# Optimization experiments

Hardware: AMD Instinct MI355X
Metric: run time of the kernel (lower is better)

The kernel has to match this reference:

```python
import jax, jax.numpy as jnp
import numpy as np

B, QL, KVL = 4, 512, 4096
Q_DIM, KV_DIM = 1024, 768
QK_CH, V_CH, H = 1024, 1024, 8
DQK, DV = QK_CH // H, V_CH // H
LN_EPS = 1e-3  # keras LayerNormalization default epsilon


def layernorm(x, gamma, beta):
    mu = jnp.mean(x, axis=-1, keepdims=True)
    var = jnp.mean(jnp.square(x - mu), axis=-1, keepdims=True)
    return (x - mu) * jax.lax.rsqrt(var + LN_EPS) * gamma + beta


def setup_inputs() -> dict:
    key = jax.random.key(0)
    ks = jax.random.split(key, 8)
    s_q = 1.0 / np.sqrt(Q_DIM)
    s_kv = 1.0 / np.sqrt(KV_DIM)
    return {
        "hidden_states": jax.random.normal(ks[0], (B, QL, Q_DIM), jnp.float32),
        "inputs": jax.random.normal(ks[1], (B, KVL, KV_DIM), jnp.float32),
        "ln1_g": jnp.ones((Q_DIM,), jnp.float32),
        "ln1_b": jnp.zeros((Q_DIM,), jnp.float32),
        "ln2_g": jnp.ones((KV_DIM,), jnp.float32),
        "ln2_b": jnp.zeros((KV_DIM,), jnp.float32),
        "Wq": jax.random.normal(ks[2], (Q_DIM, QK_CH), jnp.float32) * s_q,
        "bq": jnp.zeros((QK_CH,), jnp.float32),
        "Wk": jax.random.normal(ks[3], (KV_DIM, QK_CH), jnp.float32) * s_kv,
        "bk": jnp.zeros((QK_CH,), jnp.float32),
        "Wv": jax.random.normal(ks[4], (KV_DIM, V_CH), jnp.float32) * s_kv,
        "bv": jnp.zeros((V_CH,), jnp.float32),
    }


def reference(hidden_states, inputs, ln1_g, ln1_b, ln2_g, ln2_b, Wq, bq, Wk, bk, Wv, bv):
    # LayerNorm latents and inputs (cross-attention path)
    hs = layernorm(hidden_states, ln1_g, ln1_b)   # [B, QL, Q_DIM]
    inp = layernorm(inputs, ln2_g, ln2_b)         # [B, KVL, KV_DIM]

    q = hs @ Wq + bq                               # [B, QL, QK_CH]
    k = inp @ Wk + bk                              # [B, KVL, QK_CH]
    v = inp @ Wv + bv                              # [B, KVL, V_CH]

    q = q.reshape(B, QL, H, DQK)
    k = k.reshape(B, KVL, H, DQK)
    v = v.reshape(B, KVL, H, DV)

    scores = jnp.einsum("bqhd,bkhd->bhqk", q, k) / jnp.sqrt(jnp.asarray(DQK, q.dtype))
    probs = jax.nn.softmax(scores, axis=-1)        # [B, H, QL, KVL]
    ctx = jnp.einsum("bhqk,bkhd->bqhd", probs, v)  # [B, QL, H, DV]
    return ctx.reshape(B, QL, H * DV)
```

## Files before the change

kernel.cpp:

```cpp
#include <hip/hip_runtime.h>
#include <hip/hip_bf16.h>
#include <stdint.h>

#define B_    4
#define QL_   512
#define KVL_  4096
#define QDIM  1024
#define KVDIM 768
#define NCH   1024
#define H_    8
#define DH    128
#define NROWS (B_ * H_ * QL_)
#define KVBLK 64
#define NS    4

typedef unsigned short ushort_t;
typedef __attribute__((ext_vector_type(8))) short bf16x8;
typedef __attribute__((ext_vector_type(4))) float f32x4;
typedef __attribute__((ext_vector_type(4))) unsigned short us4;

__device__ __forceinline__ ushort_t f2bf(float x){
  union { float f; unsigned u; } v; v.f = x;
  unsigned r = v.u + 0x7FFF + ((v.u >> 16) & 1);
  return (ushort_t)(r >> 16);
}

__device__ __forceinline__ float bf2f(unsigned hs){
  union { unsigned u; float f; } v; v.u = hs << 16; return v.f;
}

__device__ __forceinline__ void gload16(void* l, const void* g){
  __builtin_amdgcn_global_load_lds(
    (const __attribute__((address_space(1))) unsigned int*)g,
    (__attribute__((address_space(3))) unsigned int*)l, 16, 0, 0);
}

template<int D>
__global__ void ln_kernel(const float* __restrict__ x, const float* __restrict__ gamma,
                          const float* __restrict__ beta, ushort_t* __restrict__ out){
  constexpr int NW = D / 256;
  int row = blockIdx.x;
  const f32x4* xr = (const f32x4*)(x + (size_t)row * D);
  int tid = threadIdx.x;
  f32x4 v = xr[tid];
  float s  = v[0] + v[1] + v[2] + v[3];
  float s2 = v[0]*v[0] + v[1]*v[1] + v[2]*v[2] + v[3]*v[3];
  #pragma unroll
  for (int m = 32; m; m >>= 1){ s += __shfl_xor(s, m); s2 += __shfl_xor(s2, m); }
  __shared__ float red[2 * NW];
  int w = tid >> 6;
  if ((tid & 63) == 0){ red[w] = s; red[NW + w] = s2; }
  __syncthreads();
  s = 0.f; s2 = 0.f;
  #pragma unroll
  for (int i = 0; i < NW; ++i){ s += red[i]; s2 += red[NW + i]; }
  float mu  = s / D;
  float var = s2 / D - mu * mu;
  float rs  = rsqrtf(var + 1e-3f);
  f32x4 gm = ((const f32x4*)gamma)[tid];
  f32x4 bt = ((const f32x4*)beta)[tid];
  us4 o;
  #pragma unroll
  for (int e = 0; e < 4; ++e) o[e] = f2bf((v[e] - mu) * rs * gm[e] + bt[e]);
  ((us4*)(out + (size_t)row * D))[tid] = o;
}

__global__ void wtrans_kernel(const float* __restrict__ W, ushort_t* __restrict__ Wt,
                              int K, int N){
  __shared__ float t[32][33];
  int n0 = blockIdx.x * 32, k0 = blockIdx.y * 32;
  int tx = threadIdx.x & 31, ty = threadIdx.x >> 5;
  #pragma unroll
  for (int i = 0; i < 32; i += 8) t[ty + i][tx] = W[(size_t)(k0 + ty + i) * N + n0 + tx];
  __syncthreads();
  #pragma unroll
  for (int i = 0; i < 32; i += 8)
    Wt[(size_t)(n0 + ty + i) * K + k0 + tx] = f2bf(t[tx][ty + i]);
}

__global__ __launch_bounds__(256)
void gemm_kernel(const ushort_t* __restrict__ A, const ushort_t* __restrict__ Bw,
                 const float* __restrict__ bias, ushort_t* __restrict__ out,
                 int M, int K, float oscale){
  __shared__ __align__(16) ushort_t lds[3][2][4][128][8];
  int tid = threadIdx.x;
  int w = tid >> 6, lane = tid & 63;
  int m0 = blockIdx.x * 128, n0 = blockIdx.y * 128;
  int wr = w >> 1, wc = w & 1;
  int g = lane >> 4, j = lane & 15;
  f32x4 acc[4][4] = {};
  const int ksteps = K / 32;
  const ushort_t* Aw  = A  + (size_t)(m0 + lane) * K + w * 8;
  const ushort_t* Bww = Bw + (size_t)(n0 + lane) * K + w * 8;

  auto stage = [&](int buf, int ks){
    #pragma unroll
    for (int i = 0; i < 2; ++i){
      gload16(&lds[buf][0][w][i*64][0], Aw  + (size_t)i*64*K + ks*32);
      gload16(&lds[buf][1][w][i*64][0], Bww + (size_t)i*64*K + ks*32);
    }
  };

  stage(0, 0);
  stage(1, 1);
  asm volatile("s_waitcnt vmcnt(4)" ::: "memory");
  __builtin_amdgcn_s_barrier();
  __builtin_amdgcn_sched_barrier(0);

  int cur = 0;
  for (int ks = 0; ks < ksteps; ++ks){
    int nxt = cur + 2; if (nxt >= 3) nxt -= 3;
    bool pf = (ks + 2 < ksteps);
    if (pf) stage(nxt, ks + 2);
    bf16x8 af[4], bfr[4];
    #pragma unroll
    for (int mi = 0; mi < 4; ++mi) af[mi]  = *(const bf16x8*)&lds[cur][0][g][wr*64 + mi*16 + j][0];
    #pragma unroll
    for (int ni = 0; ni < 4; ++ni) bfr[ni] = *(const bf16x8*)&lds[cur][1][g][wc*64 + ni*16 + j][0];
    __builtin_amdgcn_s_setprio(1);
    #pragma unroll
    for (int mi = 0; mi < 4; ++mi)
      #pragma unroll
      for (int ni = 0; ni < 4; ++ni)
        acc[mi][ni] = __builtin_amdgcn_mfma_f32_16x16x32_bf16(af[mi], bfr[ni], acc[mi][ni], 0, 0, 0);
    __builtin_amdgcn_s_setprio(0);
    if (pf) asm volatile("s_waitcnt vmcnt(4)" ::: "memory");
    else    asm volatile("s_waitcnt vmcnt(0)" ::: "memory");
    __builtin_amdgcn_s_barrier();
    __builtin_amdgcn_sched_barrier(0);
    cur += 1; if (cur >= 3) cur -= 3;
  }

  #pragma unroll
  for (int mi = 0; mi < 4; ++mi){
    int row0 = m0 + wr*64 + mi*16 + g*4;
    #pragma unroll
    for (int ni = 0; ni < 4; ++ni){
      int col = n0 + wc*64 + ni*16 + j;
      float bs = bias[col];
      #pragma unroll
      for (int r = 0; r < 4; ++r)
        out[(size_t)(row0 + r) * NCH + col] = f2bf((acc[mi][ni][r] + bs) * oscale);
    }
  }
}

template<bool TRANSV>
__global__ __launch_bounds__(512, 2)
void gemm256_kernel(const ushort_t* __restrict__ A, const ushort_t* __restrict__ Bw,
                    const float* __restrict__ bias, ushort_t* __restrict__ out,
                    int M, int K, float oscale){
  __shared__ __align__(16) ushort_t lds[3][2][256][32];
  int tid = threadIdx.x;
  int w = tid >> 6, lane = tid & 63;
  int m0 = blockIdx.x * 256, n0 = blockIdx.y * 256;
  int wr = w >> 2, wc = w & 3;
  int g = lane >> 4, j = lane & 15;
  f32x4 acc[8][4] = {};
  const int ksteps = K / 32;
  int srow = tid >> 2;
  int cg = (tid & 3) ^ ((tid >> 3) & 3);
  const ushort_t* Asrc = A  + (size_t)(m0 + srow) * K + cg * 8;
  const ushort_t* Bsrc = Bw + (size_t)(n0 + srow) * K + cg * 8;

  auto stage = [&](int buf, int ks){
    char* la = (char*)&lds[buf][0][0][0] + tid * 16;
    char* lb = (char*)&lds[buf][1][0][0] + tid * 16;
    #pragma unroll
    for (int i = 0; i < 2; ++i){
      gload16(la + i*8192, Asrc + (size_t)(i*128)*K + ks*32);
      gload16(lb + i*8192, Bsrc + (size_t)(i*128)*K + ks*32);
    }
  };

  stage(0, 0);
  stage(1, 1);
  asm volatile("s_waitcnt vmcnt(4)" ::: "memory");
  __builtin_amdgcn_s_barrier();
  __builtin_amdgcn_sched_barrier(0);

  const int swx = (g ^ ((j >> 1) & 3)) << 4;
  int cur = 0;
  for (int ks = 0; ks < ksteps; ++ks){
    int nxt = cur + 2; if (nxt >= 3) nxt -= 3;
    bool pf = (ks + 2 < ksteps);
    if (pf) stage(nxt, ks + 2);
    const char* La = (const char*)&lds[cur][0][0][0];
    const char* Lb = (const char*)&lds[cur][1][0][0];
    bf16x8 af[8], bfr[4];
    #pragma unroll
    for (int mi = 0; mi < 8; ++mi) af[mi]  = *(const bf16x8*)(La + ((wr*128 + mi*16 + j) << 6) + swx);
    #pragma unroll
    for (int ni = 0; ni < 4; ++ni) bfr[ni] = *(const bf16x8*)(Lb + ((wc*64  + ni*16 + j) << 6) + swx);
    __builtin_amdgcn_s_setprio(1);
    #pragma unroll
    for (int mi = 0; mi < 8; ++mi)
      #pragma unroll
      for (int ni = 0; ni < 4; ++ni)
        acc[mi][ni] = __builtin_amdgcn_mfma_f32_16x16x32_bf16(af[mi], bfr[ni], acc[mi][ni], 0, 0, 0);
    __builtin_amdgcn_s_setprio(0);
    if (pf) asm volatile("s_waitcnt vmcnt(4)" ::: "memory");
    else    asm volatile("s_waitcnt vmcnt(0)" ::: "memory");
    __builtin_amdgcn_s_barrier();
    __builtin_amdgcn_sched_barrier(0);
    cur += 1; if (cur >= 3) cur -= 3;
  }

  #pragma unroll
  for (int mi = 0; mi < 8; ++mi){
    int row0 = m0 + wr*128 + mi*16 + g*4;
    #pragma unroll
    for (int ni = 0; ni < 4; ++ni){
      int col = n0 + wc*64 + ni*16 + j;
      float bs = bias[col];
      if (!TRANSV){
        #pragma unroll
        for (int r = 0; r < 4; ++r)
          out[(size_t)(row0 + r) * NCH + col] = f2bf((acc[mi][ni][r] + bs) * oscale);
      } else {
        int bidx = row0 >> 12, kv = row0 & (KVL_ - 1);
        int h = col >> 7, dv = col & 127;
        int c = (kv & ~31) | (((kv & 15) >> 2) << 3) | (((kv >> 4) & 1) << 2);
        us4 pk;
        #pragma unroll
        for (int r = 0; r < 4; ++r) pk[r] = f2bf(acc[mi][ni][r] + bs);
        *(us4*)&out[((size_t)(bidx * H_ + h) * DH + dv) * KVL_ + c] = pk;
      }
    }
  }
}

__global__ __launch_bounds__(256, 2)
void attn_kernel(const ushort_t* __restrict__ Q, const ushort_t* __restrict__ Km,
                 const ushort_t* __restrict__ Vt, ushort_t* __restrict__ ctxp,
                 float* __restrict__ mlp){
  __shared__ __align__(16) ushort_t Kbuf[2][KVBLK][DH];
  __shared__ __align__(16) ushort_t Vbuf[2][DH][KVBLK];

  int bid = blockIdx.x;
  int xcd = bid & 7, slot = bid >> 3;
  int p   = xcd + 8 * (slot >> 2);
  int qb  = slot & 3;
  int bh  = p >> 2, sp = p & 3;
  int b = bh >> 3, h = bh & 7;

  int tid = threadIdx.x;
  int w = tid >> 6, lane = tid & 63;
  int g = lane >> 4, j = lane & 15;
  int qbase = qb * 128 + w * 32;

  bf16x8 qreg[2][4];
  #pragma unroll
  for (int qg = 0; qg < 2; ++qg){
    const ushort_t* Qb = Q + (size_t)(b * QL_ + qbase + qg * 16 + j) * NCH + h * DH + g * 8;
    #pragma unroll
    for (int kb = 0; kb < 4; ++kb) qreg[qg][kb] = *(const bf16x8*)(Qb + kb * 32);
  }

  f32x4 ctx[2][8] = {};
  f32x4 lacc[2] = {};
  float m_[2] = {-1e30f, -1e30f};

  const short ONEB = (short)0x3F80;
  const bf16x8 ones = {ONEB, ONEB, ONEB, ONEB, ONEB, ONEB, ONEB, ONEB};

  const int kvbeg = sp * (KVL_ / NS);
  const char* Kg = (const char*)(Km + (size_t)b * KVL_ * NCH) + h * 256;
  const char* Vg = (const char*)(Vt + (size_t)(b * H_ + h) * DH * KVL_);

  auto stage = [&](int bi, int kv0){
    #pragma unroll
    for (int i = 0; i < 4; ++i){
      int lin = (i * 256 + tid) * 16;
      int sw  = lin ^ (((lin >> 8) & 7) << 4);
      gload16((char*)&Kbuf[bi][0][0] + lin,
              Kg + (size_t)(kv0 + (sw >> 8)) * 2048 + (sw & 255));
    }
    #pragma unroll
    for (int i = 0; i < 4; ++i){
      int lin = (i * 256 + tid) * 16;
      int sw  = lin ^ (((lin >> 7) & 7) << 4);
      gload16((char*)&Vbuf[bi][0][0] + lin,
              Vg + (size_t)(sw >> 7) * (KVL_ * 2) + kv0 * 2 + (sw & 127));
    }
  };

  const float THR = 11.5415603f;
  const int NCHUNK = (KVL_ / NS) / KVBLK;

  stage(0, kvbeg);
  __syncthreads();

  for (int c = 0; c < NCHUNK; ++c){
    int bi = c & 1;
    if (c + 1 < NCHUNK) stage(bi ^ 1, kvbeg + (c + 1) * KVBLK);

    const char* Kl = (const char*)&Kbuf[bi][0][0];
    const char* Vl = (const char*)&Vbuf[bi][0][0];

    f32x4 s[2][4] = {};
    __builtin_amdgcn_s_setprio(1);
    #pragma unroll
    for (int kf = 0; kf < 4; ++kf){
      #pragma unroll
      for (int kb = 0; kb < 4; ++kb){
        int off = (kf * 16 + j) * 256 + kb * 64 + g * 16;
        off ^= ((j & 7) << 4);
        bf16x8 kfrag = *(const bf16x8*)(Kl + off);
        s[0][kf] = __builtin_amdgcn_mfma_f32_16x16x32_bf16(kfrag, qreg[0][kb], s[0][kf], 0, 0, 0);
        s[1][kf] = __builtin_amdgcn_mfma_f32_16x16x32_bf16(kfrag, qreg[1][kb], s[1][kf], 0, 0, 0);
      }
    }
    __builtin_amdgcn_s_setprio(0);

    union { unsigned u[4]; bf16x8 v; } pa[2][2];
    #pragma unroll
    for (int qg = 0; qg < 2; ++qg){
      float t0 = fmaxf(fmaxf(s[qg][0][0], s[qg][0][1]), fmaxf(s[qg][0][2], s[qg][0][3]));
      float t1 = fmaxf(fmaxf(s[qg][1][0], s[qg][1][1]), fmaxf(s[qg][1][2], s[qg][1][3]));
      float t2 = fmaxf(fmaxf(s[qg][2][0], s[qg][2][1]), fmaxf(s[qg][2][2], s[qg][2][3]));
      float t3 = fmaxf(fmaxf(s[qg][3][0], s[qg][3][1]), fmaxf(s[qg][3][2], s[qg][3][3]));
      float pm = fmaxf(fmaxf(t0, t1), fmaxf(t2, t3));
      pm = fmaxf(pm, __shfl_xor(pm, 16));
      pm = fmaxf(pm, __shfl_xor(pm, 32));
      int ok = (pm - m_[qg] <= THR);
      if (!__all(ok)){
        float mn = fmaxf(m_[qg], pm);
        float cf = exp2f(m_[qg] - mn);
        m_[qg] = mn;
        float cfr[4];
        #pragma unroll
        for (int r = 0; r < 4; ++r) cfr[r] = __shfl(cf, g * 4 + r);
        #pragma unroll
        for (int df = 0; df < 8; ++df)
          #pragma unroll
          for (int r = 0; r < 4; ++r) ctx[qg][df][r] *= cfr[r];
        #pragma unroll
        for (int r = 0; r < 4; ++r) lacc[qg][r] *= cfr[r];
      }
      #pragma unroll
      for (int kf = 0; kf < 4; ++kf)
        #pragma unroll
        for (int r = 0; r < 4; ++r)
          s[qg][kf][r] = exp2f(s[qg][kf][r] - m_[qg]);
      #pragma unroll
      for (int kb = 0; kb < 2; ++kb){
        asm("v_cvt_pk_bf16_f32 %0, %1, %2" : "=v"(pa[qg][kb].u[0]) : "v"(s[qg][2*kb][0]),   "v"(s[qg][2*kb][1]));
        asm("v_cvt_pk_bf16_f32 %0, %1, %2" : "=v"(pa[qg][kb].u[1]) : "v"(s[qg][2*kb][2]),   "v"(s[qg][2*kb][3]));
        asm("v_cvt_pk_bf16_f32 %0, %1, %2" : "=v"(pa[qg][kb].u[2]) : "v"(s[qg][2*kb+1][0]), "v"(s[qg][2*kb+1][1]));
        asm("v_cvt_pk_bf16_f32 %0, %1, %2" : "=v"(pa[qg][kb].u[3]) : "v"(s[qg][2*kb+1][2]), "v"(s[qg][2*kb+1][3]));
      }
    }

    __builtin_amdgcn_s_setprio(1);
    lacc[0] = __builtin_amdgcn_mfma_f32_16x16x32_bf16(pa[0][0].v, ones, lacc[0], 0, 0, 0);
    lacc[0] = __builtin_amdgcn_mfma_f32_16x16x32_bf16(pa[0][1].v, ones, lacc[0], 0, 0, 0);
    lacc[1] = __builtin_amdgcn_mfma_f32_16x16x32_bf16(pa[1][0].v, ones, lacc[1], 0, 0, 0);
    lacc[1] = __builtin_amdgcn_mfma_f32_16x16x32_bf16(pa[1][1].v, ones, lacc[1], 0, 0, 0);
    #pragma unroll
    for (int df = 0; df < 8; ++df){
      int off0 = (df * 16 + j) * 128 + g * 16;        int o0 = off0 ^ ((j & 7) << 4);
      int off1 = (df * 16 + j) * 128 + 64 + g * 16;   int o1 = off1 ^ ((j & 7) << 4);
      bf16x8 v0 = *(const bf16x8*)(Vl + o0);
      bf16x8 v1 = *(const bf16x8*)(Vl + o1);
      ctx[0][df] = __builtin_amdgcn_mfma_f32_16x16x32_bf16(pa[0][0].v, v0, ctx[0][df], 0, 0, 0);
      ctx[0][df] = __builtin_amdgcn_mfma_f32_16x16x32_bf16(pa[0][1].v, v1, ctx[0][df], 0, 0, 0);
      ctx[1][df] = __builtin_amdgcn_mfma_f32_16x16x32_bf16(pa[1][0].v, v0, ctx[1][df], 0, 0, 0);
      ctx[1][df] = __builtin_amdgcn_mfma_f32_16x16x32_bf16(pa[1][1].v, v1, ctx[1][df], 0, 0, 0);
    }
    __builtin_amdgcn_s_setprio(0);
    __syncthreads();
  }

  #pragma unroll
  for (int qg = 0; qg < 2; ++qg){
    size_t prow0 = ((size_t)sp * 32 + bh) * QL_ + qbase + qg * 16;
    #pragma unroll
    for (int r = 0; r < 4; ++r){
      ushort_t* cp = ctxp + (prow0 + g * 4 + r) * DH;
      #pragma unroll
      for (int df = 0; df < 8; ++df) cp[df * 16 + j] = f2bf(ctx[qg][df][r]);
    }
    if (j == 0){
      #pragma unroll
      for (int r = 0; r < 4; ++r)
        mlp[(prow0 + g * 4 + r) * 2 + 1] = lacc[qg][r];
    }
    if (g == 0)
      mlp[(prow0 + j) * 2] = m_[qg];
  }
}

__global__ __launch_bounds__(256)
void combine_kernel(const ushort_t* __restrict__ ctxp, const float* __restrict__ mlp,
                    float* __restrict__ out){
  int row = blockIdx.x * 4 + (threadIdx.x >> 6);
  int lane = threadIdx.x & 63;
  int b = row >> 12, h = (row >> 9) & 7, q = row & 511;
  float ms[NS], ls[NS];
  #pragma unroll
  for (int s = 0; s < NS; ++s){
    ms[s] = mlp[((size_t)(s * NROWS + row)) * 2];
    ls[s] = mlp[((size_t)(s * NROWS + row)) * 2 + 1];
  }
  float M = ms[0];
  #pragma unroll
  for (int s = 1; s < NS; ++s) M = fmaxf(M, ms[s]);
  float wgt[NS], L = 0.f;
  #pragma unroll
  for (int s = 0; s < NS; ++s){ wgt[s] = exp2f(ms[s] - M); L += ls[s] * wgt[s]; }
  float inv = 1.f / L;
  float ax = 0.f, ay = 0.f;
  #pragma unroll
  for (int s = 0; s < NS; ++s){
    unsigned pk = *(const unsigned*)(ctxp + ((size_t)(s * NROWS + row)) * DH + lane * 2);
    ax += bf2f(pk & 0xFFFFu) * wgt[s];
    ay += bf2f(pk >> 16) * wgt[s];
  }
  float* op = out + ((size_t)(b * QL_ + q)) * NCH + h * DH + lane * 2;
  op[0] = ax * inv; op[1] = ay * inv;
}

extern "C" void kernel_launch(void* const* d_in, const int* in_sizes, int n_in,
                              void* d_out, int out_size, void* d_ws, size_t ws_size,
                              hipStream_t stream){
  const float* hs   = (const float*)d_in[0];
  const float* inp  = (const float*)d_in[1];
  const float* ln1g = (const float*)d_in[2];
  const float* ln1b = (const float*)d_in[3];
  const float* ln2g = (const float*)d_in[4];
  const float* ln2b = (const float*)d_in[5];
  const float* Wq   = (const float*)d_in[6];
  const float* bq   = (const float*)d_in[7];
  const float* Wk   = (const float*)d_in[8];
  const float* bk   = (const float*)d_in[9];
  const float* Wv   = (const float*)d_in[10];
  const float* bv   = (const float*)d_in[11];

  char* ws = (char*)d_ws;
  size_t off = 0;
  auto alloc = [&](size_t bytes){ void* pp = ws + off; off += (bytes + 255) & ~255ull; return pp; };
  ushort_t* Qm = (ushort_t*)alloc((size_t)2048 * 1024 * 2);
  ushort_t* Km = (ushort_t*)alloc((size_t)16384 * 1024 * 2);
  ushort_t* Vt = (ushort_t*)alloc((size_t)16384 * 1024 * 2);
  size_t base2 = off;
  ushort_t* hs_ln = (ushort_t*)alloc((size_t)2048 * 1024 * 2);
  ushort_t* in_ln = (ushort_t*)alloc((size_t)16384 * 768 * 2);
  ushort_t* Wqt   = (ushort_t*)alloc((size_t)1024 * 1024 * 2);
  ushort_t* Wkt   = (ushort_t*)alloc((size_t)1024 * 768 * 2);
  ushort_t* Wvt   = (ushort_t*)alloc((size_t)1024 * 768 * 2);
  off = base2;
  ushort_t* ctxp = (ushort_t*)alloc((size_t)NS * NROWS * DH * 2);
  float*    mlp  = (float*)alloc((size_t)NS * NROWS * 2 * 4);

  const float QSC = 0.08838834764831845f * 1.4426950408889634f;

  ln_kernel<1024><<<2048, 256, 0, stream>>>(hs, ln1g, ln1b, hs_ln);
  ln_kernel<768><<<16384, 192, 0, stream>>>(inp, ln2g, ln2b, in_ln);
  wtrans_kernel<<<dim3(32, 32), 256, 0, stream>>>(Wq, Wqt, 1024, 1024);
  wtrans_kernel<<<dim3(32, 24), 256, 0, stream>>>(Wk, Wkt, 768, 1024);
  wtrans_kernel<<<dim3(32, 24), 256, 0, stream>>>(Wv, Wvt, 768, 1024);
  gemm_kernel<<<dim3(16, 8), 256, 0, stream>>>(hs_ln, Wqt, bq, Qm, 2048, 1024, QSC);
  gemm256_kernel<false><<<dim3(64, 4), 512, 0, stream>>>(in_ln, Wkt, bk, Km, 16384, 768, 1.0f);
  gemm256_kernel<true ><<<dim3(64, 4), 512, 0, stream>>>(in_ln, Wvt, bv, Vt, 16384, 768, 1.0f);
  attn_kernel<<<512, 256, 0, stream>>>(Qm, Km, Vt, ctxp, mlp);
  combine_kernel<<<NROWS / 4, 256, 0, stream>>>(ctxp, mlp, (float*)d_out);
}
```

Measured before the change: 169.8 us.

## Load GEMM B-operand and attention V fragments directly from global into registers

In the projection GEMM, the weight (B) tile is no longer staged through LDS. Each wave loads its B fragments straight from global memory into registers, one k-step ahead, and LDS now holds only the A tile. In the attention kernel, the V tile is no longer staged in shared memory. Each wave reads its V fragments from global memory at the start of every chunk. This removes LDS traffic and footprint, but every wave now loads the shared B/V data redundantly. The V loads are issued only one phase ahead, so global latency can stall the PV MFMAs, and the hand-set vmcnt waits become more fragile.

```diff
diff --git a/kernel.cpp b/kernel.cpp
--- a/kernel.cpp
+++ b/kernel.cpp
@@ -150,7 +150,7 @@
 void gemm256_kernel(const ushort_t* __restrict__ A, const ushort_t* __restrict__ Bw,
                     const float* __restrict__ bias, ushort_t* __restrict__ out,
                     int M, int K, float oscale){
-  __shared__ __align__(16) ushort_t lds[3][2][256][32];
+  __shared__ __align__(16) ushort_t lds[3][256][32];
   int tid = threadIdx.x;
   int w = tid >> 6, lane = tid & 63;
   int m0 = blockIdx.x * 256, n0 = blockIdx.y * 256;
@@ -160,22 +160,27 @@
   const int ksteps = K / 32;
   int srow = tid >> 2;
   int cg = (tid & 3) ^ ((tid >> 3) & 3);
-  const ushort_t* Asrc = A  + (size_t)(m0 + srow) * K + cg * 8;
-  const ushort_t* Bsrc = Bw + (size_t)(n0 + srow) * K + cg * 8;
+  const ushort_t* Asrc = A + (size_t)(m0 + srow) * K + cg * 8;
+  const ushort_t* Bn   = Bw + (size_t)(n0 + wc * 64 + j) * K + g * 8;
 
   auto stage = [&](int buf, int ks){
-    char* la = (char*)&lds[buf][0][0][0] + tid * 16;
-    char* lb = (char*)&lds[buf][1][0][0] + tid * 16;
-    #pragma unroll
-    for (int i = 0; i < 2; ++i){
+    char* la = (char*)&lds[buf][0][0] + tid * 16;
+    #pragma unroll
+    for (int i = 0; i < 2; ++i)
       gload16(la + i*8192, Asrc + (size_t)(i*128)*K + ks*32);
-      gload16(lb + i*8192, Bsrc + (size_t)(i*128)*K + ks*32);
-    }
   };
 
+  auto loadB = [&](bf16x8* d, int ks){
+    #pragma unroll
+    for (int ni = 0; ni < 4; ++ni)
+      d[ni] = *(const bf16x8*)(Bn + (size_t)(ni*16)*K + ks*32);
+  };
+
+  bf16x8 bcur[4], bnxt[4];
   stage(0, 0);
   stage(1, 1);
-  asm volatile("s_waitcnt vmcnt(4)" ::: "memory");
+  loadB(bcur, 0);
+  asm volatile("s_waitcnt vmcnt(2)" ::: "memory");
   __builtin_amdgcn_s_barrier();
   __builtin_amdgcn_sched_barrier(0);
 
@@ -185,21 +190,21 @@
     int nxt = cur + 2; if (nxt >= 3) nxt -= 3;
     bool pf = (ks + 2 < ksteps);
     if (pf) stage(nxt, ks + 2);
-    const char* La = (const char*)&lds[cur][0][0][0];
-    const char* Lb = (const char*)&lds[cur][1][0][0];
-    bf16x8 af[8], bfr[4];
-    #pragma unroll
-    for (int mi = 0; mi < 8; ++mi) af[mi]  = *(const bf16x8*)(La + ((wr*128 + mi*16 + j) << 6) + swx);
-    #pragma unroll
-    for (int ni = 0; ni < 4; ++ni) bfr[ni] = *(const bf16x8*)(Lb + ((wc*64  + ni*16 + j) << 6) + swx);
+    if (ks + 1 < ksteps) loadB(bnxt, ks + 1);
+    const char* La = (const char*)&lds[cur][0][0];
+    bf16x8 af[8];
+    #pragma unroll
+    for (int mi = 0; mi < 8; ++mi) af[mi] = *(const bf16x8*)(La + ((wr*128 + mi*16 + j) << 6) + swx);
     __builtin_amdgcn_s_setprio(1);
     #pragma unroll
     for (int mi = 0; mi < 8; ++mi)
       #pragma unroll
       for (int ni = 0; ni < 4; ++ni)
-        acc[mi][ni] = __builtin_amdgcn_mfma_f32_16x16x32_bf16(af[mi], bfr[ni], acc[mi][ni], 0, 0, 0);
+        acc[mi][ni] = __builtin_amdgcn_mfma_f32_16x16x32_bf16(af[mi], bcur[ni], acc[mi][ni], 0, 0, 0);
     __builtin_amdgcn_s_setprio(0);
-    if (pf) asm volatile("s_waitcnt vmcnt(4)" ::: "memory");
+    #pragma unroll
+    for (int ni = 0; ni < 4; ++ni) bcur[ni] = bnxt[ni];
+    if (pf) asm volatile("s_waitcnt vmcnt(2)" ::: "memory");
     else    asm volatile("s_waitcnt vmcnt(0)" ::: "memory");
     __builtin_amdgcn_s_barrier();
     __builtin_amdgcn_sched_barrier(0);
@@ -235,7 +240,6 @@
                  const ushort_t* __restrict__ Vt, ushort_t* __restrict__ ctxp,
                  float* __restrict__ mlp){
   __shared__ __align__(16) ushort_t Kbuf[2][KVBLK][DH];
-  __shared__ __align__(16) ushort_t Vbuf[2][DH][KVBLK];
 
   int bid = blockIdx.x;
   int xcd = bid & 7, slot = bid >> 3;
@@ -266,7 +270,7 @@
 
   const int kvbeg = sp * (KVL_ / NS);
   const char* Kg = (const char*)(Km + (size_t)b * KVL_ * NCH) + h * 256;
-  const char* Vg = (const char*)(Vt + (size_t)(b * H_ + h) * DH * KVL_);
+  const ushort_t* Vb = Vt + ((size_t)(b * H_ + h) * DH + j) * KVL_ + g * 8;
 
   auto stage = [&](int bi, int kv0){
     #pragma unroll
@@ -276,13 +280,6 @@
       gload16((char*)&Kbuf[bi][0][0] + lin,
               Kg + (size_t)(kv0 + (sw >> 8)) * 2048 + (sw & 255));
     }
-    #pragma unroll
-    for (int i = 0; i < 4; ++i){
-      int lin = (i * 256 + tid) * 16;
-      int sw  = lin ^ (((lin >> 7) & 7) << 4);
-      gload16((char*)&Vbuf[bi][0][0] + lin,
-              Vg + (size_t)(sw >> 7) * (KVL_ * 2) + kv0 * 2 + (sw & 127));
-    }
   };
 
   const float THR = 11.5415603f;
@@ -293,10 +290,18 @@
 
   for (int c = 0; c < NCHUNK; ++c){
     int bi = c & 1;
-    if (c + 1 < NCHUNK) stage(bi ^ 1, kvbeg + (c + 1) * KVBLK);
+    int kv0 = kvbeg + c * KVBLK;
+    if (c + 1 < NCHUNK) stage(bi ^ 1, kv0 + KVBLK);
+
+    bf16x8 vf[8][2];
+    #pragma unroll
+    for (int df = 0; df < 8; ++df){
+      #pragma unroll
+      for (int kc = 0; kc < 2; ++kc)
+        vf[df][kc] = *(const bf16x8*)(Vb + (size_t)(df * 16) * KVL_ + kv0 + kc * 32);
+    }
 
     const char* Kl = (const char*)&Kbuf[bi][0][0];
-    const char* Vl = (const char*)&Vbuf[bi][0][0];
 
     f32x4 s[2][4] = {};
     __builtin_amdgcn_s_setprio(1);
@@ -359,14 +364,10 @@
     lacc[1] = __builtin_amdgcn_mfma_f32_16x16x32_bf16(pa[1][1].v, ones, lacc[1], 0, 0, 0);
     #pragma unroll
     for (int df = 0; df < 8; ++df){
-      int off0 = (df * 16 + j) * 128 + g * 16;        int o0 = off0 ^ ((j & 7) << 4);
-      int off1 = (df * 16 + j) * 128 + 64 + g * 16;   int o1 = off1 ^ ((j & 7) << 4);
-      bf16x8 v0 = *(const bf16x8*)(Vl + o0);
-      bf16x8 v1 = *(const bf16x8*)(Vl + o1);
-      ctx[0][df] = __builtin_amdgcn_mfma_f32_16x16x32_bf16(pa[0][0].v, v0, ctx[0][df], 0, 0, 0);
-      ctx[0][df] = __builtin_amdgcn_mfma_f32_16x16x32_bf16(pa[0][1].v, v1, ctx[0][df], 0, 0, 0);
-      ctx[1][df] = __builtin_amdgcn_mfma_f32_16x16x32_bf16(pa[1][0].v, v0, ctx[1][df], 0, 0, 0);
-      ctx[1][df] = __builtin_amdgcn_mfma_f32_16x16x32_bf16(pa[1][1].v, v1, ctx[1][df], 0, 0, 0);
+      ctx[0][df] = __builtin_amdgcn_mfma_f32_16x16x32_bf16(pa[0][0].v, vf[df][0], ctx[0][df], 0, 0, 0);
+      ctx[0][df] = __builtin_amdgcn_mfma_f32_16x16x32_bf16(pa[0][1].v, vf[df][1], ctx[0][df], 0, 0, 0);
+      ctx[1][df] = __builtin_amdgcn_mfma_f32_16x16x32_bf16(pa[1][0].v, vf[df][0], ctx[1][df], 0, 0, 0);
+      ctx[1][df] = __builtin_amdgcn_mfma_f32_16x16x32_bf16(pa[1][1].v, vf[df][1], ctx[1][df], 0, 0, 0);
     }
     __builtin_amdgcn_s_setprio(0);
     __syncthreads();
```

Measured after the change: 227.3 us. 1.34x slower.
